# Optimization experiments

Measured on AMD Instinct MI355X. Metric: run time of the kernel, lower is better.

## Reference

```python
import jax, jax.numpy as jnp
import numpy as np

NUM_CAPSULES = 10
NUM_ROUTES = 512
IN_CHANNELS = 8
OUT_CHANNELS = 16
BATCH = 512  # must equal NUM_ROUTES for the module's broadcast to be valid


def squash(x):
    # norm over last dim; v = ||s||^2/(1+||s||^2) * s/||s||
    norm = jnp.linalg.norm(x, axis=-1, keepdims=True)
    norm_sq = norm ** 2
    return norm_sq / (1.0 + norm_sq) * (x / norm)


def setup_inputs() -> dict:
    key = jax.random.key(0)
    k1, k2 = jax.random.split(key)
    x = jax.random.normal(k1, (BATCH, NUM_ROUTES, IN_CHANNELS), dtype=jnp.float32)
    route_weights = jax.random.normal(
        k2, (NUM_CAPSULES, NUM_ROUTES, IN_CHANNELS, OUT_CHANNELS), dtype=jnp.float32
    )
    return {"x": x, "route_weights": route_weights}


def reference(x, route_weights):
    B, R, Cin = x.shape
    # x -> [B, 1, R, Cin] (after view/unsqueeze/permute in the torch code)
    xb = x[:, None, :, :]
    # route_weights.permute(1,0,2,3) -> [R, num_caps, Cin, Cout]
    w = jnp.transpose(route_weights, (1, 0, 2, 3))
    # torch/jnp matmul broadcast of batch dims (B,1) vs (R,num_caps); B==R here.
    # u_hat[b, j] = x[b] @ w[route=b, cap=j]  -> [B, num_caps, R, Cout]
    u_hat = jnp.matmul(xb, w)
    b_ij = jnp.zeros(u_hat.shape[:3] + (1,), dtype=u_hat.dtype)
    for _ in range(3):  # fixed 3 routing iterations
        c_ij = jax.nn.softmax(b_ij, axis=2)            # softmax over routes
        s_j = jnp.sum(c_ij * u_hat, axis=2, keepdims=True)  # [B,J,1,Cout]
        v_j = squash(s_j)
        b_ij = b_ij + jnp.sum(u_hat * v_j, axis=-1, keepdims=True)
    return jnp.squeeze(v_j, axis=2)  # [B, num_caps, Cout]
```

## Files before the change

kernel.cpp:

```cpp
#include <hip/hip_runtime.h>
#include <math.h>

constexpr int BATCH = 512;
constexpr int NC    = 10;
constexpr int RR    = 512;
constexpr int CI    = 8;
constexpr int CO    = 16;

constexpr int TPB = 64;
constexpr int RPT = RR / TPB;

__global__ __launch_bounds__(TPB) void caps_route_kernel(
    const float* __restrict__ x,
    const float* __restrict__ rw,
    float* __restrict__ out)
{
    const int blk  = blockIdx.x;
    const int b    = blk / NC;
    const int c    = blk - b * NC;
    const int t    = threadIdx.x;

    __shared__ __align__(16) float W[CI][CO];

    {
        const size_t base = ((size_t)c * RR + b) * (CI * CO);
        ((float*)W)[t]      = rw[base + t];
        ((float*)W)[t + 64] = rw[base + t + 64];
    }
    __syncthreads();

    float xs[RPT][CI];
    #pragma unroll
    for (int k = 0; k < RPT; ++k) {
        const float4* xp = (const float4*)(x + ((size_t)b * RR + t + k * TPB) * CI);
        float4 a0 = xp[0], a1 = xp[1];
        xs[k][0]=a0.x; xs[k][1]=a0.y; xs[k][2]=a0.z; xs[k][3]=a0.w;
        xs[k][4]=a1.x; xs[k][5]=a1.y; xs[k][6]=a1.z; xs[k][7]=a1.w;
    }

    float logit[RPT];
    #pragma unroll
    for (int k = 0; k < RPT; ++k) logit[k] = 0.f;

    float num[CO];
    float ks = 0.f;

    for (int iter = 0; iter < 3; ++iter) {
        float yl[CI];
        float den = 0.f;
        if (iter == 0) {
            #pragma unroll
            for (int i = 0; i < CI; ++i) {
                float a = (xs[0][i] + xs[1][i]) + (xs[2][i] + xs[3][i]);
                float d = (xs[4][i] + xs[5][i]) + (xs[6][i] + xs[7][i]);
                yl[i] = a + d;
            }
        } else {
            float e[RPT];
            #pragma unroll
            for (int k = 0; k < RPT; ++k) e[k] = __expf(logit[k]);
            den = ((e[0] + e[1]) + (e[2] + e[3])) + ((e[4] + e[5]) + (e[6] + e[7]));
            #pragma unroll
            for (int i = 0; i < CI; ++i) {
                float a = fmaf(e[0], xs[0][i], e[1] * xs[1][i]);
                float d = fmaf(e[2], xs[2][i], e[3] * xs[3][i]);
                float f = fmaf(e[4], xs[4][i], e[5] * xs[5][i]);
                float g = fmaf(e[6], xs[6][i], e[7] * xs[7][i]);
                yl[i] = (a + d) + (f + g);
            }
        }

        float s1[4];
        {
            const bool hi = (t & 32) != 0;
            #pragma unroll
            for (int k = 0; k < 4; ++k) {
                float keep = hi ? yl[4 + k] : yl[k];
                float send = hi ? yl[k]     : yl[4 + k];
                s1[k] = keep + __shfl_xor(send, 32, 64);
            }
        }
        float s2[2];
        {
            const bool hi = (t & 16) != 0;
            #pragma unroll
            for (int k = 0; k < 2; ++k) {
                float keep = hi ? s1[2 + k] : s1[k];
                float send = hi ? s1[k]     : s1[2 + k];
                s2[k] = keep + __shfl_xor(send, 16, 64);
            }
        }
        float s3;
        {
            const bool hi = (t & 8) != 0;
            float keep = hi ? s2[1] : s2[0];
            float send = hi ? s2[0] : s2[1];
            s3 = keep + __shfl_xor(send, 8, 64);
        }
        s3 += __shfl_xor(s3, 4, 64);
        s3 += __shfl_xor(s3, 2, 64);
        s3 += __shfl_xor(s3, 1, 64);

        if (iter != 0) {
            den += __shfl_xor(den, 32, 64);
            den += __shfl_xor(den, 16, 64);
            den += __shfl_xor(den,  8, 64);
            den += __shfl_xor(den,  4, 64);
            den += __shfl_xor(den,  2, 64);
            den += __shfl_xor(den,  1, 64);
        } else {
            den = (float)RR;
        }

        float y[CI];
        #pragma unroll
        for (int i = 0; i < CI; ++i)
            y[i] = __shfl(s3, i << 3, 64);

        {
            float4 a0 = make_float4(0.f,0.f,0.f,0.f);
            float4 a1 = a0, a2 = a0, a3 = a0;
            #pragma unroll
            for (int i = 0; i < CI; ++i) {
                const float4* Wr = (const float4*)&W[i][0];
                float4 w0 = Wr[0], w1 = Wr[1], w2 = Wr[2], w3 = Wr[3];
                const float yi = y[i];
                a0.x = fmaf(yi, w0.x, a0.x); a0.y = fmaf(yi, w0.y, a0.y);
                a0.z = fmaf(yi, w0.z, a0.z); a0.w = fmaf(yi, w0.w, a0.w);
                a1.x = fmaf(yi, w1.x, a1.x); a1.y = fmaf(yi, w1.y, a1.y);
                a1.z = fmaf(yi, w1.z, a1.z); a1.w = fmaf(yi, w1.w, a1.w);
                a2.x = fmaf(yi, w2.x, a2.x); a2.y = fmaf(yi, w2.y, a2.y);
                a2.z = fmaf(yi, w2.z, a2.z); a2.w = fmaf(yi, w2.w, a2.w);
                a3.x = fmaf(yi, w3.x, a3.x); a3.y = fmaf(yi, w3.y, a3.y);
                a3.z = fmaf(yi, w3.z, a3.z); a3.w = fmaf(yi, w3.w, a3.w);
            }
            num[0]=a0.x; num[1]=a0.y; num[2]=a0.z; num[3]=a0.w;
            num[4]=a1.x; num[5]=a1.y; num[6]=a1.z; num[7]=a1.w;
            num[8]=a2.x; num[9]=a2.y; num[10]=a2.z; num[11]=a2.w;
            num[12]=a3.x; num[13]=a3.y; num[14]=a3.z; num[15]=a3.w;
        }

        const float inv = 1.0f / den;

        #pragma unroll
        for (int o = 0; o < CO; ++o) num[o] *= inv;

        float nsq = 0.f;
        #pragma unroll
        for (int o = 0; o < CO; ++o) nsq = fmaf(num[o], num[o], nsq);
        const float nrm = sqrtf(nsq);
        ks = nrm / (1.0f + nsq);

        if (iter < 2) {
            float wv[CI];
            #pragma unroll
            for (int i = 0; i < CI; ++i) {
                const float4* Wr = (const float4*)&W[i][0];
                float4 w0 = Wr[0], w1 = Wr[1], w2 = Wr[2], w3 = Wr[3];
                float d0 = fmaf(w0.x, num[0],  w0.y * num[1]);
                float d1 = fmaf(w0.z, num[2],  w0.w * num[3]);
                float d2 = fmaf(w1.x, num[4],  w1.y * num[5]);
                float d3 = fmaf(w1.z, num[6],  w1.w * num[7]);
                float d4 = fmaf(w2.x, num[8],  w2.y * num[9]);
                float d5 = fmaf(w2.z, num[10], w2.w * num[11]);
                float d6 = fmaf(w3.x, num[12], w3.y * num[13]);
                float d7 = fmaf(w3.z, num[14], w3.w * num[15]);
                wv[i] = ((d0 + d1) + (d2 + d3)) + ((d4 + d5) + (d6 + d7));
            }
            #pragma unroll
            for (int k = 0; k < RPT; ++k) {
                float d = 0.f;
                #pragma unroll
                for (int i = 0; i < CI; ++i) d = fmaf(xs[k][i], wv[i], d);
                logit[k] = fmaf(d, ks, logit[k]);
            }
        }
    }

    if (t < 4) {
        float4* op = (float4*)(out + ((size_t)b * NC + c) * CO);
        op[t] = make_float4(num[4*t+0]*ks, num[4*t+1]*ks,
                            num[4*t+2]*ks, num[4*t+3]*ks);
    }
}

extern "C" void kernel_launch(void* const* d_in, const int* in_sizes, int n_in,
                              void* d_out, int out_size, void* d_ws, size_t ws_size,
                              hipStream_t stream) {
    const float* x  = (const float*)d_in[0];
    const float* rw = (const float*)d_in[1];
    float* out = (float*)d_out;

    dim3 grid(BATCH * NC);
    dim3 block(TPB);
    caps_route_kernel<<<grid, block, 0, stream>>>(x, rw, out);
}
```

Before: 24.76 us.

## Precompute per-route Gram matrices of weights to shrink routing-loop math

Adds a first kernel that computes the 8x8 Gram matrix W·Wᵀ for each (batch, capsule) pair and stores it in the workspace. The routing kernel then works in the 8-dim input space: the squash norm and the agreement vector come from G·z, and the 16-wide output is formed only once at the end. This cuts the per-iteration matvecs against the 8x16 weight block, but adds a second kernel launch and a workspace round trip of 64 floats per block. G is read from global memory with uniform addresses, and the old single-kernel path is kept as a fallback when the workspace is too small.

```diff
diff --git a/kernel.cpp b/kernel.cpp
--- a/kernel.cpp
+++ b/kernel.cpp
@@ -10,18 +10,184 @@
 constexpr int TPB = 64;
 constexpr int RPT = RR / TPB;
 
-__global__ __launch_bounds__(TPB) void caps_route_kernel(
+__global__ __launch_bounds__(TPB) void caps_gram_kernel(
+    const float* __restrict__ rw,
+    float* __restrict__ Gws)
+{
+    const int blk = blockIdx.x;
+    const int b   = blk / NC;
+    const int c   = blk - b * NC;
+    const int t   = threadIdx.x;
+
+    __shared__ __align__(16) float W[CI * CO];
+    const float* Wg = rw + ((size_t)c * RR + b) * (CI * CO);
+    W[t]      = Wg[t];
+    W[t + 64] = Wg[t + 64];
+    __syncthreads();
+
+    const int i = t >> 3;
+    const int j = t & 7;
+    const float4* ri = (const float4*)&W[i * CO];
+    const float4* rj = (const float4*)&W[j * CO];
+    float acc = 0.f;
+    #pragma unroll
+    for (int q = 0; q < 4; ++q) {
+        float4 a = ri[q], d = rj[q];
+        acc = fmaf(a.x, d.x, acc);
+        acc = fmaf(a.y, d.y, acc);
+        acc = fmaf(a.z, d.z, acc);
+        acc = fmaf(a.w, d.w, acc);
+    }
+    Gws[(size_t)blk * 64 + t] = acc;
+}
+
+__global__ __launch_bounds__(TPB) void caps_route_g_kernel(
     const float* __restrict__ x,
     const float* __restrict__ rw,
+    const float* __restrict__ Gws,
     float* __restrict__ out)
 {
-    const int blk  = blockIdx.x;
-    const int b    = blk / NC;
-    const int c    = blk - b * NC;
-    const int t    = threadIdx.x;
+    const int blk = blockIdx.x;
+    const int b   = blk / NC;
+    const int c   = blk - b * NC;
+    const int t   = threadIdx.x;
+
+    const float* __restrict__ G = Gws + (size_t)blk * 64;
+
+    float xs[RPT][CI];
+    #pragma unroll
+    for (int k = 0; k < RPT; ++k) {
+        const float4* xp = (const float4*)(x + ((size_t)b * RR + t + k * TPB) * CI);
+        float4 a0 = xp[0], a1 = xp[1];
+        xs[k][0]=a0.x; xs[k][1]=a0.y; xs[k][2]=a0.z; xs[k][3]=a0.w;
+        xs[k][4]=a1.x; xs[k][5]=a1.y; xs[k][6]=a1.z; xs[k][7]=a1.w;
+    }
+
+    float logit[RPT];
+    #pragma unroll
+    for (int k = 0; k < RPT; ++k) logit[k] = 0.f;
+
+    float z[CI];
+    float ks = 0.f;
+
+    for (int iter = 0; iter < 3; ++iter) {
+        float yl[CI];
+        float den = 0.f;
+        if (iter == 0) {
+            #pragma unroll
+            for (int i = 0; i < CI; ++i) {
+                float a = (xs[0][i] + xs[1][i]) + (xs[2][i] + xs[3][i]);
+                float d = (xs[4][i] + xs[5][i]) + (xs[6][i] + xs[7][i]);
+                yl[i] = a + d;
+            }
+        } else {
+            float e[RPT];
+            #pragma unroll
+            for (int k = 0; k < RPT; ++k) e[k] = __expf(logit[k]);
+            den = ((e[0] + e[1]) + (e[2] + e[3])) + ((e[4] + e[5]) + (e[6] + e[7]));
+            #pragma unroll
+            for (int i = 0; i < CI; ++i) {
+                float a = fmaf(e[0], xs[0][i], e[1] * xs[1][i]);
+                float d = fmaf(e[2], xs[2][i], e[3] * xs[3][i]);
+                float f = fmaf(e[4], xs[4][i], e[5] * xs[5][i]);
+                float g = fmaf(e[6], xs[6][i], e[7] * xs[7][i]);
+                yl[i] = (a + d) + (f + g);
+            }
+        }
+
+        float s1[4];
+        {
+            const bool hi = (t & 32) != 0;
+            #pragma unroll
+            for (int k = 0; k < 4; ++k) {
+                float keep = hi ? yl[4 + k] : yl[k];
+                float send = hi ? yl[k]     : yl[4 + k];
+                s1[k] = keep + __shfl_xor(send, 32, 64);
+            }
+        }
+        float s2[2];
+        {
+            const bool hi = (t & 16) != 0;
+            #pragma unroll
+            for (int k = 0; k < 2; ++k) {
+                float keep = hi ? s1[2 + k] : s1[k];
+                float send = hi ? s1[k]     : s1[2 + k];
+                s2[k] = keep + __shfl_xor(send, 16, 64);
+            }
+        }
+        float s3;
+        {
+            const bool hi = (t & 8) != 0;
+            float keep = hi ? s2[1] : s2[0];
+            float send = hi ? s2[0] : s2[1];
+            s3 = keep + __shfl_xor(send, 8, 64);
+        }
+        s3 += __shfl_xor(s3, 4, 64);
+        s3 += __shfl_xor(s3, 2, 64);
+        s3 += __shfl_xor(s3, 1, 64);
+
+        if (iter != 0) {
+            den += __shfl_xor(den, 32, 64);
+            den += __shfl_xor(den, 16, 64);
+            den += __shfl_xor(den,  8, 64);
+            den += __shfl_xor(den,  4, 64);
+            den += __shfl_xor(den,  2, 64);
+            den += __shfl_xor(den,  1, 64);
+        } else {
+            den = (float)RR;
+        }
+
+        const float inv = 1.0f / den;
+        #pragma unroll
+        for (int i = 0; i < CI; ++i)
+            z[i] = __shfl(s3, i << 3, 64) * inv;
+
+        float g[CI];
+        #pragma unroll
+        for (int i = 0; i < CI; ++i) {
+            float d0 = fmaf(G[i*8+0], z[0], G[i*8+1] * z[1]);
+            float d1 = fmaf(G[i*8+2], z[2], G[i*8+3] * z[3]);
+            float d2 = fmaf(G[i*8+4], z[4], G[i*8+5] * z[5]);
+            float d3 = fmaf(G[i*8+6], z[6], G[i*8+7] * z[7]);
+            g[i] = (d0 + d1) + (d2 + d3);
+        }
+        float nsq = 0.f;
+        #pragma unroll
+        for (int i = 0; i < CI; ++i) nsq = fmaf(z[i], g[i], nsq);
+        const float nrm = sqrtf(nsq);
+        ks = nrm / (1.0f + nsq);
+
+        if (iter < 2) {
+            #pragma unroll
+            for (int k = 0; k < RPT; ++k) {
+                float d = 0.f;
+                #pragma unroll
+                for (int i = 0; i < CI; ++i) d = fmaf(xs[k][i], g[i], d);
+                logit[k] = fmaf(d, ks, logit[k]);
+            }
+        }
+    }
+
+    if (t < CO) {
+        const float* Wg = rw + ((size_t)c * RR + b) * (CI * CO);
+        float val = 0.f;
+        #pragma unroll
+        for (int i = 0; i < CI; ++i)
+            val = fmaf(z[i], Wg[i * CO + t], val);
+        out[((size_t)b * NC + c) * CO + t] = val * ks;
+    }
+}
+
+__global__ __launch_bounds__(TPB) void caps_route_lds_kernel(
+    const float* __restrict__ x, const float* __restrict__ rw,
+    float* __restrict__ out)
+{
+    const int blk = blockIdx.x;
+    const int b   = blk / NC;
+    const int c   = blk - b * NC;
+    const int t   = threadIdx.x;
 
     __shared__ __align__(16) float W[CI][CO];
-
     {
         const size_t base = ((size_t)c * RR + b) * (CI * CO);
         ((float*)W)[t]      = rw[base + t];
@@ -141,7 +307,6 @@
         }
 
         const float inv = 1.0f / den;
-
         #pragma unroll
         for (int o = 0; o < CO; ++o) num[o] *= inv;
 
@@ -191,7 +356,15 @@
     const float* rw = (const float*)d_in[1];
     float* out = (float*)d_out;
 
+    const size_t g_bytes = (size_t)BATCH * NC * 64 * sizeof(float);
     dim3 grid(BATCH * NC);
     dim3 block(TPB);
-    caps_route_kernel<<<grid, block, 0, stream>>>(x, rw, out);
+
+    if (ws_size >= g_bytes) {
+        float* Gws = (float*)d_ws;
+        caps_gram_kernel<<<grid, block, 0, stream>>>(rw, Gws);
+        caps_route_g_kernel<<<grid, block, 0, stream>>>(x, rw, Gws, out);
+    } else {
+        caps_route_lds_kernel<<<grid, block, 0, stream>>>(x, rw, out);
+    }
 }
```

After: 25.43 us. 1.03x slower.
